# Performance work log

Hardware: AMD Instinct MI355X
Metric: run time of the kernel (lower is better)

The kernel has to match this reference:

```python
import jax, jax.numpy as jnp
import numpy as np

N, IN_DIM, HID, H = 4096, 128, 512, 8
D = HID // H  # head_dim = 64
NEG = -1e9


def setup_inputs() -> dict:
    key = jax.random.key(0)
    ks = jax.random.split(key, 16)
    s_in = 1.0 / np.sqrt(IN_DIM)
    s_h = 1.0 / np.sqrt(HID)
    return {
        "node_features": jax.random.normal(ks[0], (N, IN_DIM), jnp.float32),
        "edge_mask_bool": jax.random.bernoulli(ks[1], 0.3, (1, 1, N, N)),
        "time_bias": jax.random.normal(ks[2], (1, 1, N, N), jnp.float32) * 0.1,
        "W_in": jax.random.normal(ks[3], (IN_DIM, HID), jnp.float32) * s_in,
        "b_in": jnp.zeros((HID,), jnp.float32),
        "Wq": jax.random.normal(ks[4], (HID, HID), jnp.float32) * s_h,
        "bq": jnp.zeros((HID,), jnp.float32),
        "Wk": jax.random.normal(ks[5], (HID, HID), jnp.float32) * s_h,
        "bk": jnp.zeros((HID,), jnp.float32),
        "Wv": jax.random.normal(ks[6], (HID, HID), jnp.float32) * s_h,
        "bv": jnp.zeros((HID,), jnp.float32),
        "Wo": jax.random.normal(ks[7], (HID, HID), jnp.float32) * s_h,
        "bo": jnp.zeros((HID,), jnp.float32),
    }


def reference(node_features, edge_mask_bool, time_bias, W_in, b_in, Wq, bq, Wk, bk, Wv, bv, Wo, bo):
    # input projection + QKV projections
    x = node_features @ W_in + b_in                       # [N, HID]
    q = (x @ Wq + bq).reshape(N, H, D)                    # [N, H, D]
    k = (x @ Wk + bk).reshape(N, H, D)
    v = (x @ Wv + bv).reshape(N, H, D)
    # scores [H, N, N], scaled by sqrt(head_dim)
    scores = jnp.einsum("nhd,mhd->hnm", q, k) / jnp.sqrt(jnp.asarray(D, x.dtype))
    # additive mask: True blocks attention (-1e9), plus time bias
    bias = edge_mask_bool[0, 0].astype(x.dtype) * NEG + time_bias[0, 0]  # [N, N]
    scores = scores + bias[None, :, :]
    attn = jax.nn.softmax(scores, axis=-1)                # [H, N, N]
    out = jnp.einsum("hnm,mhd->nhd", attn, v).reshape(N, HID)
    return out @ Wo + bo                                  # [N, HID]
```

## Files before the change

### kernel.cpp

```cpp
#include <hip/hip_runtime.h>
#include <hip/hip_bf16.h>

static constexpr int kN   = 4096;
static constexpr int kIn  = 128;
static constexpr int kHid = 512;
static constexpr int kH   = 8;
static constexpr int kD   = 64;
#define MASKF (-30000.0f)

static constexpr int kKFS = 32768 + 64;
static constexpr int kVFS = 131072 + 64;

typedef __bf16    bf16x8 __attribute__((ext_vector_type(8)));
typedef _Float16  f16x8  __attribute__((ext_vector_type(8)));
typedef unsigned short u16x8 __attribute__((ext_vector_type(8)));
typedef float  f32x4  __attribute__((ext_vector_type(4)));
typedef float  f32x16 __attribute__((ext_vector_type(16)));

__device__ __forceinline__ unsigned short f2bf(float f) {
    return __builtin_bit_cast(unsigned short, (__bf16)f);
}
__device__ __forceinline__ unsigned pkbf(float a, float b) {
    return (unsigned)f2bf(a) | ((unsigned)f2bf(b) << 16);
}
__device__ __forceinline__ unsigned short f2h(float f) {
    return __builtin_bit_cast(unsigned short, (_Float16)f);
}

__global__ void misc_kernel(const unsigned int* __restrict__ m, int* __restrict__ mode,
                            const float* __restrict__ bq, const float* __restrict__ bk,
                            const float* __restrict__ bv, float* __restrict__ dst,
                            const float* __restrict__ W_in, unsigned short* __restrict__ Wb_in) {
    if (blockIdx.x < 6) {
        int i = blockIdx.x * 256 + threadIdx.x;
        dst[i] = i < 512 ? bq[i] : (i < 1024 ? bk[i - 512] : bv[i - 1024]);
        return;
    }
    if (blockIdx.x == 6) {
        int t = threadIdx.x;
        if (t >= 64) return;
        int isf = 0, isb = 0;
        for (int i = t; i < 4096; i += 64) {
            unsigned int w = m[i];
            if (w == 0x3F800000u) isf = 1;
            else if (w > 1u)      isb = 1;
        }
        unsigned long long bf = __ballot(isf != 0);
        unsigned long long bb = __ballot(isb != 0);
        if (t == 0) mode[0] = bf ? 2 : (bb ? 1 : 0);
        return;
    }
    int i = (blockIdx.x - 7) * 256 + threadIdx.x;
    if (i < kIn * kHid) Wb_in[i] = f2bf(W_in[i]);
}

__global__ __launch_bounds__(256) void prepass_kernel(const void* __restrict__ maskp,
                                                      const float* __restrict__ tb,
                                                      const int* __restrict__ modep,
                                                      unsigned short* __restrict__ bc) {
    const int mode = modep[0];
    size_t idx = ((size_t)blockIdx.x * 256 + threadIdx.x) * 8;
    float tv[8];
    *(float4*)&tv[0] = *(const float4*)(tb + idx);
    *(float4*)&tv[4] = *(const float4*)(tb + idx + 4);
    u16x8 o;
    if (mode == 0) {
        const int* mp = (const int*)maskp;
        int4 a = *(const int4*)(mp + idx);
        int4 b = *(const int4*)(mp + idx + 4);
        int mv[8] = {a.x, a.y, a.z, a.w, b.x, b.y, b.z, b.w};
#pragma unroll
        for (int j = 0; j < 8; j++) o[j] = f2h(mv[j] ? MASKF : tv[j]);
    } else if (mode == 1) {
        const unsigned char* mp = (const unsigned char*)maskp;
        uint2 u = *(const uint2*)(mp + idx);
#pragma unroll
        for (int j = 0; j < 4; j++) o[j] = f2h(((u.x >> (8 * j)) & 255u) ? MASKF : tv[j]);
#pragma unroll
        for (int j = 0; j < 4; j++) o[4 + j] = f2h(((u.y >> (8 * j)) & 255u) ? MASKF : tv[4 + j]);
    } else {
        const float* mp = (const float*)maskp;
        float4 a = *(const float4*)(mp + idx);
        float4 b = *(const float4*)(mp + idx + 4);
        float mv[8] = {a.x, a.y, a.z, a.w, b.x, b.y, b.z, b.w};
#pragma unroll
        for (int j = 0; j < 8; j++) o[j] = f2h((mv[j] != 0.f) ? MASKF : tv[j]);
    }
    *(u16x8*)(bc + idx) = o;
}

__global__ void transpose_all_kernel(const float* __restrict__ s0, const float* __restrict__ s1,
                                     const float* __restrict__ s2, const float* __restrict__ s3,
                                     unsigned short* __restrict__ d0, unsigned short* __restrict__ d1,
                                     unsigned short* __restrict__ d2, unsigned short* __restrict__ d3) {
    __shared__ float t[32][33];
    int z = blockIdx.z;
    const float* src = z == 0 ? s0 : z == 1 ? s1 : z == 2 ? s2 : s3;
    unsigned short* dst = z == 0 ? d0 : z == 1 ? d1 : z == 2 ? d2 : d3;
    int c0 = blockIdx.x * 32, r0 = blockIdx.y * 32;
    int tx = threadIdx.x, ty = threadIdx.y;
#pragma unroll
    for (int i = 0; i < 4; i++) {
        int r = ty + i * 8;
        t[r][tx] = src[(size_t)(r0 + r) * kHid + c0 + tx];
    }
    __syncthreads();
#pragma unroll
    for (int i = 0; i < 4; i++) {
        int r = ty + i * 8;
        dst[(size_t)(c0 + r) * kHid + r0 + tx] = f2bf(t[tx][r]);
    }
}

__global__ __launch_bounds__(256) void bc_kernel(const float* __restrict__ b_in,
                                                 const unsigned short* __restrict__ Wt_qkv,
                                                 const float* __restrict__ bqkv,
                                                 float* __restrict__ bc) {
    int j = blockIdx.x * 256 + threadIdx.x;
    float acc = bqkv[j];
    const unsigned short* row = Wt_qkv + (size_t)j * kHid;
    for (int i0 = 0; i0 < kHid; i0 += 8) {
        bf16x8 wv = *(const bf16x8*)(row + i0);
#pragma unroll
        for (int k = 0; k < 8; k++) acc += b_in[i0 + k] * (float)wv[k];
    }
    bc[j] = acc;
}

template <bool ABF, int OMODE>
__global__ __launch_bounds__(256) void gemm_kernel(const void* __restrict__ Ap,
                                                   const unsigned short* __restrict__ Bt,
                                                   const float* __restrict__ bias,
                                                   void* __restrict__ Cp, void* __restrict__ Cp2,
                                                   void* __restrict__ Cp3,
                                                   int M, int Nn, int K, int ldc) {
    __shared__ unsigned short As[128][40];
    __shared__ unsigned short Bs[128][40];
    const int tid  = threadIdx.x;
    const int lane = tid & 63;
    const int wv   = tid >> 6;
    const int wr   = wv >> 1, wc = wv & 1;
    const int m0 = blockIdx.x * 128, n0 = blockIdx.y * 128;
    const int g = lane >> 4, li = lane & 15;

    f32x4 acc[4][4] = {};
    const int rr = tid >> 2;
    const int cc = (tid & 3) * 8;

    for (int k0 = 0; k0 < K; k0 += 32) {
#pragma unroll
        for (int p = 0; p < 128; p += 64) {
            int r = rr + p;
            if (ABF) {
                const unsigned short* A = (const unsigned short*)Ap;
                *(uint4*)&As[r][cc] = *(const uint4*)(A + (size_t)(m0 + r) * K + k0 + cc);
            } else {
                const float* A = (const float*)Ap;
                const float4 v0 = *(const float4*)(A + (size_t)(m0 + r) * K + k0 + cc);
                const float4 v1 = *(const float4*)(A + (size_t)(m0 + r) * K + k0 + cc + 4);
                uint4 u;
                u.x = f2bf(v0.x) | ((unsigned)f2bf(v0.y) << 16);
                u.y = f2bf(v0.z) | ((unsigned)f2bf(v0.w) << 16);
                u.z = f2bf(v1.x) | ((unsigned)f2bf(v1.y) << 16);
                u.w = f2bf(v1.z) | ((unsigned)f2bf(v1.w) << 16);
                *(uint4*)&As[r][cc] = u;
            }
            *(uint4*)&Bs[r][cc] = *(const uint4*)(Bt + (size_t)(n0 + r) * K + k0 + cc);
        }
        __syncthreads();

        bf16x8 af[4], bfv[4];
#pragma unroll
        for (int mi = 0; mi < 4; mi++)
            af[mi] = *(const bf16x8*)&As[wr * 64 + mi * 16 + li][g * 8];
#pragma unroll
        for (int ni = 0; ni < 4; ni++)
            bfv[ni] = *(const bf16x8*)&Bs[wc * 64 + ni * 16 + li][g * 8];
#pragma unroll
        for (int mi = 0; mi < 4; mi++)
#pragma unroll
            for (int ni = 0; ni < 4; ni++)
                acc[mi][ni] = __builtin_amdgcn_mfma_f32_16x16x32_bf16(af[mi], bfv[ni], acc[mi][ni], 0, 0, 0);
        __syncthreads();
    }

#pragma unroll
    for (int mi = 0; mi < 4; mi++) {
        int rowb = m0 + wr * 64 + mi * 16 + g * 4;
#pragma unroll
        for (int ni = 0; ni < 4; ni++) {
            int col = n0 + wc * 64 + ni * 16 + li;
            float bv = bias ? bias[col] : 0.f;
            if (OMODE == 3) {
                if (col < 512) {
                    unsigned short* C = (unsigned short*)Cp;
#pragma unroll
                    for (int r2 = 0; r2 < 4; r2++)
                        C[(size_t)(rowb + r2) * 512 + col] = f2bf(acc[mi][ni][r2] + bv);
                } else if (col < 1024) {
                    int d = col - 512;
                    unsigned short* Kf = (unsigned short*)Cp2;
                    size_t base = (size_t)(d >> 3) * kKFS + (size_t)(d & 7);
#pragma unroll
                    for (int r2 = 0; r2 < 4; r2++)
                        Kf[base + ((size_t)(rowb + r2) << 3)] = f2bf(acc[mi][ni][r2] + bv);
                } else {
                    int d = col - 1024;
                    unsigned short* Vf = (unsigned short*)Cp3;
                    size_t base = (size_t)(d >> 5) * kVFS + ((size_t)(rowb >> 3) << 8) +
                                  ((size_t)(d & 31) << 3) + (size_t)(rowb & 7);
                    ushort4 st;
                    st.x = f2bf(acc[mi][ni][0] + bv);
                    st.y = f2bf(acc[mi][ni][1] + bv);
                    st.z = f2bf(acc[mi][ni][2] + bv);
                    st.w = f2bf(acc[mi][ni][3] + bv);
                    *(ushort4*)(Vf + base) = st;
                }
            } else if (OMODE == 1) {
                unsigned short* C = (unsigned short*)Cp;
#pragma unroll
                for (int r2 = 0; r2 < 4; r2++)
                    C[(size_t)(rowb + r2) * ldc + col] = f2bf(acc[mi][ni][r2] + bv);
            } else {
                float* C = (float*)Cp;
#pragma unroll
                for (int r2 = 0; r2 < 4; r2++)
                    C[(size_t)(rowb + r2) * ldc + col] = acc[mi][ni][r2] + bv;
            }
        }
    }
}

__global__ __launch_bounds__(512, 4) void attn_kernel(
    const unsigned short* __restrict__ qg, const unsigned short* __restrict__ kfb,
    const unsigned short* __restrict__ vfb,
    const unsigned short* __restrict__ bcb,
    float* __restrict__ Op, float* __restrict__ Mp, float* __restrict__ Lp,
    int KZ, int NC) {
    __shared__ float bias_s[2][128][33];

    const int tid  = threadIdx.x;
    const int lane = tid & 63;
    const int w    = tid >> 6;
    const int q5   = lane & 31;
    const int hi   = lane >> 5;
    const int n0   = blockIdx.x * 32;
    const int z    = blockIdx.y;
    const int kz0  = z * KZ;
    const int hb   = w * kD;

    bf16x8 qf[4];
#pragma unroll
    for (int f = 0; f < 4; f++)
        qf[f] = *(const bf16x8*)(qg + (size_t)(n0 + q5) * 512 + hb + f * 16 + hi * 8);

    f32x16 po[2] = {};
    float m_run = -3e38f, l_run = 0.f;

    const int sr  = tid & 31;
    const int scg = tid >> 5;
    float stg[8];

    auto stage_load = [&](int kbase) {
        size_t idx = (size_t)(n0 + sr) * kN + kbase + scg * 8;
        f16x8 v = *(const f16x8*)(bcb + idx);
#pragma unroll
        for (int j = 0; j < 8; j++) stg[j] = (float)v[j];
    };
    auto stage_write = [&](int buf) {
#pragma unroll
        for (int j = 0; j < 8; j++) bias_s[buf][scg * 8 + j][sr] = stg[j];
    };

    auto kload = [&](int kpos, int f) -> bf16x8 {
        return *(const bf16x8*)(kfb + (size_t)(w * 8 + f * 2 + hi) * kKFS + ((size_t)(kpos + q5) << 3));
    };

    stage_load(kz0);
    stage_write(0);
    __syncthreads();

    for (int c = 0; c < NC; c++) {
        if (c + 1 < NC) stage_load(kz0 + (c + 1) * 128);
        const int cb = c & 1;
        const int kbase = kz0 + c * 128;

        bf16x8 kcur[4], knxt[4];
#pragma unroll
        for (int f = 0; f < 4; f++) kcur[f] = kload(kbase, f);

#pragma unroll
        for (int s = 0; s < 4; s++) {
            const int kpos = kbase + s * 32;
            bf16x8 vb00, vb01, vb10, vb11;
            {
                const size_t v0 = (size_t)(w * 2 + 0) * kVFS + (((size_t)kpos >> 3) << 8) + ((size_t)q5 << 3);
                const size_t v1 = (size_t)(w * 2 + 1) * kVFS + (((size_t)kpos >> 3) << 8) + ((size_t)q5 << 3);
                vb00 = *(const bf16x8*)(vfb + v0 + ((size_t)hi << 8));
                vb01 = *(const bf16x8*)(vfb + v0 + ((size_t)(2 + hi) << 8));
                vb10 = *(const bf16x8*)(vfb + v1 + ((size_t)hi << 8));
                vb11 = *(const bf16x8*)(vfb + v1 + ((size_t)(2 + hi) << 8));
            }
            if (s < 3) {
#pragma unroll
                for (int f = 0; f < 4; f++) knxt[f] = kload(kbase + (s + 1) * 32, f);
            }
            f32x16 sc = {};
#pragma unroll
            for (int f = 0; f < 4; f++)
                sc = __builtin_amdgcn_mfma_f32_32x32x16_bf16(kcur[f], qf[f], sc, 0, 0, 0);

            float v[16];
#pragma unroll
            for (int r = 0; r < 16; r++) {
                int key = (r & 3) + 8 * (r >> 2) + 4 * hi;
                v[r] = fmaf(sc[r], 0.125f, bias_s[cb][s * 32 + key][q5]);
            }
            float t8[8];
#pragma unroll
            for (int i = 0; i < 8; i++) t8[i] = fmaxf(v[2 * i], v[2 * i + 1]);
#pragma unroll
            for (int i = 0; i < 4; i++) t8[i] = fmaxf(t8[i], t8[i + 4]);
            t8[0] = fmaxf(t8[0], t8[2]); t8[1] = fmaxf(t8[1], t8[3]);
            float mx = fmaxf(t8[0], t8[1]);
            mx = fmaxf(mx, __shfl_xor(mx, 32));
            if (!__all(mx <= m_run + 8.0f)) {
                float mnew = fmaxf(m_run, mx);
                float alpha = __expf(m_run - mnew);
                m_run = mnew;
                l_run *= alpha;
                po[0] *= alpha;
                po[1] *= alpha;
            }
            float p[16], s8[8];
#pragma unroll
            for (int i = 0; i < 8; i++) {
                p[2 * i]     = __expf(v[2 * i] - m_run);
                p[2 * i + 1] = __expf(v[2 * i + 1] - m_run);
                s8[i] = p[2 * i] + p[2 * i + 1];
            }
#pragma unroll
            for (int i = 0; i < 4; i++) s8[i] += s8[i + 4];
            l_run += (s8[0] + s8[2]) + (s8[1] + s8[3]);
            unsigned su[8], tu[8];
#pragma unroll
            for (int i = 0; i < 8; i++) su[i] = pkbf(p[2 * i], p[2 * i + 1]);
#pragma unroll
            for (int i = 0; i < 8; i++) tu[i] = __shfl_xor(su[i], 32);
            uint4 f0 = hi ? uint4{tu[2], tu[3], su[2], su[3]} : uint4{su[0], su[1], tu[0], tu[1]};
            uint4 f1 = hi ? uint4{tu[6], tu[7], su[6], su[7]} : uint4{su[4], su[5], tu[4], tu[5]};
            bf16x8 pf0 = __builtin_bit_cast(bf16x8, f0);
            bf16x8 pf1 = __builtin_bit_cast(bf16x8, f1);
            po[0] = __builtin_amdgcn_mfma_f32_32x32x16_bf16(vb00, pf0, po[0], 0, 0, 0);
            po[0] = __builtin_amdgcn_mfma_f32_32x32x16_bf16(vb01, pf1, po[0], 0, 0, 0);
            po[1] = __builtin_amdgcn_mfma_f32_32x32x16_bf16(vb10, pf0, po[1], 0, 0, 0);
            po[1] = __builtin_amdgcn_mfma_f32_32x32x16_bf16(vb11, pf1, po[1], 0, 0, 0);
            if (s < 3) {
#pragma unroll
                for (int f = 0; f < 4; f++) kcur[f] = knxt[f];
            }
        }
        if (c + 1 < NC) {
            __syncthreads();
            stage_write((c + 1) & 1);
            __syncthreads();
        }
    }

    l_run += __shfl_xor(l_run, 32);
    float* ob = Op + ((((size_t)z * kN + n0 + q5) * kH + w) << 6);
#pragma unroll
    for (int a = 0; a < 2; a++)
#pragma unroll
        for (int m = 0; m < 4; m++) {
            float4 st = {po[a][4 * m], po[a][4 * m + 1], po[a][4 * m + 2], po[a][4 * m + 3]};
            *(float4*)(ob + a * 32 + 8 * m + 4 * hi) = st;
        }
    if (lane < 32) {
        Mp[((size_t)z * kN + n0 + q5) * kH + w] = m_run;
        Lp[((size_t)z * kN + n0 + q5) * kH + w] = l_run;
    }
}

__global__ __launch_bounds__(256) void combine_kernel(const float* __restrict__ Op,
                                                      const float* __restrict__ Mp,
                                                      const float* __restrict__ Lp,
                                                      unsigned short* __restrict__ xo, int NZ) {
    int idx = blockIdx.x * 256 + threadIdx.x;
    int n = idx >> 9, c = idx & 511;
    int h = c >> 6, d = c & 63;
    float m = -3e38f;
    for (int zz = 0; zz < NZ; zz++)
        m = fmaxf(m, Mp[((size_t)zz * kN + n) * kH + h]);
    float num = 0.f, den = 0.f;
    for (int zz = 0; zz < NZ; zz++) {
        float a = __expf(Mp[((size_t)zz * kN + n) * kH + h] - m);
        den += a * Lp[((size_t)zz * kN + n) * kH + h];
        num += a * Op[(((size_t)zz * kN + n) * kH + h) * kD + d];
    }
    xo[idx] = f2bf(num / den);
}

extern "C" void kernel_launch(void* const* d_in, const int* in_sizes, int n_in,
                              void* d_out, int out_size, void* d_ws, size_t ws_size,
                              hipStream_t stream) {
    const float* node = (const float*)d_in[0];
    const void*  mask = d_in[1];
    const float* tb   = (const float*)d_in[2];
    const float* W_in = (const float*)d_in[3];
    const float* b_in = (const float*)d_in[4];
    const float* Wq   = (const float*)d_in[5];
    const float* bq   = (const float*)d_in[6];
    const float* Wk   = (const float*)d_in[7];
    const float* bk   = (const float*)d_in[8];
    const float* Wv   = (const float*)d_in[9];
    const float* bv   = (const float*)d_in[10];
    const float* Wo   = (const float*)d_in[11];
    const float* bo   = (const float*)d_in[12];
    (void)in_sizes; (void)n_in; (void)out_size;

    char* ws = (char*)d_ws;
    size_t off = 0;
    auto alloc = [&](size_t bytes) {
        void* p = ws + off;
        off += (bytes + 255) & ~(size_t)255;
        return p;
    };
    unsigned short* qb   = (unsigned short*)alloc((size_t)kN * kHid * 2);
    unsigned short* kf   = (unsigned short*)alloc((size_t)64 * kKFS * 2);
    unsigned short* vf   = (unsigned short*)alloc((size_t)16 * kVFS * 2);
    unsigned short* xo   = (unsigned short*)alloc((size_t)kN * kHid * 2);
    unsigned short* bias_c = (unsigned short*)alloc((size_t)kN * kN * 2);
    unsigned short* Wt_qkv = (unsigned short*)alloc((size_t)3 * kHid * kHid * 2);
    unsigned short* Wt_o   = (unsigned short*)alloc((size_t)kHid * kHid * 2);
    unsigned short* Wb_in  = (unsigned short*)alloc((size_t)kIn * kHid * 2);
    unsigned short* Wct    = (unsigned short*)alloc((size_t)1536 * kIn * 2);
    float* bqkv = (float*)alloc(1536 * 4);
    float* bc   = (float*)alloc(1536 * 4);
    int*   mode = (int*)alloc(256);

    size_t fixed = off;
    size_t perz = (((size_t)kN * kHid * 4 + 255) & ~(size_t)255) +
                  2 * (((size_t)kN * kH * 4 + 255) & ~(size_t)255);
    int NZ = 4;
    if (fixed + 4 * perz > ws_size) NZ = 2;
    if (fixed + 2 * perz > ws_size) NZ = 1;
    float* Op = (float*)alloc((size_t)NZ * kN * kHid * 4);
    float* Mp = (float*)alloc((size_t)NZ * kN * kH * 4);
    float* Lp = (float*)alloc((size_t)NZ * kN * kH * 4);

    misc_kernel<<<263, 256, 0, stream>>>((const unsigned int*)mask, mode, bq, bk, bv, bqkv,
                                         W_in, Wb_in);
    transpose_all_kernel<<<dim3(16, 16, 4), dim3(32, 8), 0, stream>>>(
        Wq, Wk, Wv, Wo, Wt_qkv, Wt_qkv + (size_t)kHid * kHid,
        Wt_qkv + (size_t)2 * kHid * kHid, Wt_o);
    bc_kernel<<<6, 256, 0, stream>>>(b_in, Wt_qkv, bqkv, bc);
    gemm_kernel<true, 1><<<dim3(12, 1), 256, 0, stream>>>(
        Wt_qkv, Wb_in, nullptr, Wct, nullptr, nullptr, 1536, kIn, kHid, kIn);
    prepass_kernel<<<(kN * kN) / (256 * 8), 256, 0, stream>>>(mask, tb, mode, bias_c);

    gemm_kernel<false, 3><<<dim3(kN / 128, 1536 / 128), 256, 0, stream>>>(
        node, Wct, bc, qb, kf, vf, kN, 1536, kIn, 512);

    const int KZ = kN / NZ;
    attn_kernel<<<dim3(kN / 32, NZ), 512, 0, stream>>>(
        qb, kf, vf, bias_c, Op, Mp, Lp, KZ, KZ / 128);
    combine_kernel<<<(kN * kHid) / 256, 256, 0, stream>>>(Op, Mp, Lp, xo, NZ);

    gemm_kernel<true, 0><<<dim3(kN / 128, kHid / 128), 256, 0, stream>>>(
        xo, Wt_o, bo, d_out, nullptr, nullptr, kN, kHid, kHid, kHid);
}
```

Measured before the change: 195.4 us.

## Switch softmax to base-2 exponent domain and raise key-split count to eight

Folds log2(e) into the precomputed bias and the score scale so the attention loop can use the native exp2 instruction instead of __expf, which needs an extra multiply. The mask value and the rescale threshold are converted to the log2 domain to match, and the combine kernel uses exp2 as well. It also allows up to eight key splits when the workspace has room, giving more parallel blocks at the cost of more partial output traffic in the combine step.

```diff
diff --git a/kernel.cpp b/kernel.cpp
--- a/kernel.cpp
+++ b/kernel.cpp
@@ -6,10 +6,14 @@
 static constexpr int kHid = 512;
 static constexpr int kH   = 8;
 static constexpr int kD   = 64;
-#define MASKF (-30000.0f)
 
 static constexpr int kKFS = 32768 + 64;
 static constexpr int kVFS = 131072 + 64;
+
+#define LOG2E  1.44269504f
+#define SCLG2  0.18033688f
+#define MASKL2 (-43281.0f)
+#define THRL2  11.5415603f
 
 typedef __bf16    bf16x8 __attribute__((ext_vector_type(8)));
 typedef _Float16  f16x8  __attribute__((ext_vector_type(8)));
@@ -25,6 +29,13 @@
 }
 __device__ __forceinline__ unsigned short f2h(float f) {
     return __builtin_bit_cast(unsigned short, (_Float16)f);
+}
+__device__ __forceinline__ float fast_exp2(float x) {
+#if __has_builtin(__builtin_amdgcn_exp2f)
+    return __builtin_amdgcn_exp2f(x);
+#else
+    return exp2f(x);
+#endif
 }
 
 __global__ void misc_kernel(const unsigned int* __restrict__ m, int* __restrict__ mode,
@@ -70,21 +81,21 @@
         int4 b = *(const int4*)(mp + idx + 4);
         int mv[8] = {a.x, a.y, a.z, a.w, b.x, b.y, b.z, b.w};
 #pragma unroll
-        for (int j = 0; j < 8; j++) o[j] = f2h(mv[j] ? MASKF : tv[j]);
+        for (int j = 0; j < 8; j++) o[j] = f2h(mv[j] ? MASKL2 : tv[j] * LOG2E);
     } else if (mode == 1) {
         const unsigned char* mp = (const unsigned char*)maskp;
         uint2 u = *(const uint2*)(mp + idx);
 #pragma unroll
-        for (int j = 0; j < 4; j++) o[j] = f2h(((u.x >> (8 * j)) & 255u) ? MASKF : tv[j]);
-#pragma unroll
-        for (int j = 0; j < 4; j++) o[4 + j] = f2h(((u.y >> (8 * j)) & 255u) ? MASKF : tv[4 + j]);
+        for (int j = 0; j < 4; j++) o[j] = f2h(((u.x >> (8 * j)) & 255u) ? MASKL2 : tv[j] * LOG2E);
+#pragma unroll
+        for (int j = 0; j < 4; j++) o[4 + j] = f2h(((u.y >> (8 * j)) & 255u) ? MASKL2 : tv[4 + j] * LOG2E);
     } else {
         const float* mp = (const float*)maskp;
         float4 a = *(const float4*)(mp + idx);
         float4 b = *(const float4*)(mp + idx + 4);
         float mv[8] = {a.x, a.y, a.z, a.w, b.x, b.y, b.z, b.w};
 #pragma unroll
-        for (int j = 0; j < 8; j++) o[j] = f2h((mv[j] != 0.f) ? MASKF : tv[j]);
+        for (int j = 0; j < 8; j++) o[j] = f2h((mv[j] != 0.f) ? MASKL2 : tv[j] * LOG2E);
     }
     *(u16x8*)(bc + idx) = o;
 }
@@ -314,7 +325,7 @@
 #pragma unroll
             for (int r = 0; r < 16; r++) {
                 int key = (r & 3) + 8 * (r >> 2) + 4 * hi;
-                v[r] = fmaf(sc[r], 0.125f, bias_s[cb][s * 32 + key][q5]);
+                v[r] = fmaf(sc[r], SCLG2, bias_s[cb][s * 32 + key][q5]);
             }
             float t8[8];
 #pragma unroll
@@ -324,9 +335,9 @@
             t8[0] = fmaxf(t8[0], t8[2]); t8[1] = fmaxf(t8[1], t8[3]);
             float mx = fmaxf(t8[0], t8[1]);
             mx = fmaxf(mx, __shfl_xor(mx, 32));
-            if (!__all(mx <= m_run + 8.0f)) {
+            if (!__all(mx <= m_run + THRL2)) {
                 float mnew = fmaxf(m_run, mx);
-                float alpha = __expf(m_run - mnew);
+                float alpha = fast_exp2(m_run - mnew);
                 m_run = mnew;
                 l_run *= alpha;
                 po[0] *= alpha;
@@ -335,8 +346,8 @@
             float p[16], s8[8];
 #pragma unroll
             for (int i = 0; i < 8; i++) {
-                p[2 * i]     = __expf(v[2 * i] - m_run);
-                p[2 * i + 1] = __expf(v[2 * i + 1] - m_run);
+                p[2 * i]     = fast_exp2(v[2 * i] - m_run);
+                p[2 * i + 1] = fast_exp2(v[2 * i + 1] - m_run);
                 s8[i] = p[2 * i] + p[2 * i + 1];
             }
 #pragma unroll
@@ -394,7 +405,7 @@
         m = fmaxf(m, Mp[((size_t)zz * kN + n) * kH + h]);
     float num = 0.f, den = 0.f;
     for (int zz = 0; zz < NZ; zz++) {
-        float a = __expf(Mp[((size_t)zz * kN + n) * kH + h] - m);
+        float a = fast_exp2(Mp[((size_t)zz * kN + n) * kH + h] - m);
         den += a * Lp[((size_t)zz * kN + n) * kH + h];
         num += a * Op[(((size_t)zz * kN + n) * kH + h) * kD + d];
     }
@@ -442,9 +453,8 @@
     size_t fixed = off;
     size_t perz = (((size_t)kN * kHid * 4 + 255) & ~(size_t)255) +
                   2 * (((size_t)kN * kH * 4 + 255) & ~(size_t)255);
-    int NZ = 4;
-    if (fixed + 4 * perz > ws_size) NZ = 2;
-    if (fixed + 2 * perz > ws_size) NZ = 1;
+    int NZ = 8;
+    while (NZ > 1 && fixed + (size_t)NZ * perz > ws_size) NZ >>= 1;
     float* Op = (float*)alloc((size_t)NZ * kN * kHid * 4);
     float* Mp = (float*)alloc((size_t)NZ * kN * kH * 4);
     float* Lp = (float*)alloc((size_t)NZ * kN * kH * 4);
```

Result: slower. 213.9 us (+9.5%).
